# Kernel tuning notes

Hardware: AMD Instinct MI355X
Metric: run time of the kernel (lower is better)

Reference implementation:

```python
import jax, jax.numpy as jnp
import numpy as np

INPUT_DIM = 16
LW = 128          # layerwidth
NB_LAYERS = 4
NB_X = 4096
NB_THETA = 128
PARAM_COUNT = INPUT_DIM * LW + LW + (NB_LAYERS - 1) * (LW * LW + LW) + LW + 1  # 51841


def setup_inputs() -> dict:
    k1, k2 = jax.random.split(jax.random.key(0))
    x = jax.random.normal(k1, (NB_X, INPUT_DIM), dtype=jnp.float32)
    theta = jax.random.normal(k2, (NB_THETA, PARAM_COUNT), dtype=jnp.float32)
    return {"x": x, "theta": theta}


def reference(x, theta):
    # x: [nb_x, input_dim], theta: [nb_theta, param_count]
    t = theta.shape[0]
    off = 0
    # first layer: W0 [t, LW, INPUT_DIM], b0 [t, LW]
    W0 = theta[:, off:off + INPUT_DIM * LW].reshape(t, LW, INPUT_DIM); off += INPUT_DIM * LW
    b0 = theta[:, off:off + LW]; off += LW
    h = jnp.tanh(jnp.einsum('thi,xi->txh', W0, x) + b0[:, None, :])  # [t, nb_x, LW]
    # hidden layers
    for _ in range(NB_LAYERS - 1):
        W = theta[:, off:off + LW * LW].reshape(t, LW, LW); off += LW * LW
        b = theta[:, off:off + LW]; off += LW
        h = jnp.tanh(jnp.einsum('tho,txo->txh', W, h) + b[:, None, :])
    # output layer: Wl [t, LW], bl [t, 1]
    Wl = theta[:, off:off + LW]; off += LW
    bl = theta[:, off:off + 1]
    out = jnp.einsum('th,txh->tx', Wl, h)[..., None] + bl[:, None, :]  # [t, nb_x, 1]
    return out
```

## Files before the change

### kernel.cpp

```cpp
#include <hip/hip_runtime.h>


#define IND      16
#define THREADS  1024
#define PARAMS   51841
#define SCALE    2.8853900817779268f

#define WS_W0    12582912
#define WS_SC    (WS_W0 + 128 * 8192)
#define WS_X     (WS_SC + 128 * 4096)
#define WS_XLO   (WS_X + 131072)
#define WS_TOTAL (WS_X + 262144)


#define LDS_B    98304
#define LDS_WL   (LDS_B + 1536)
#define LDS_SZ   (LDS_B + 2064)

typedef _Float16 f16x8 __attribute__((ext_vector_type(8)));
typedef _Float16 f16x4 __attribute__((ext_vector_type(4)));
typedef float    f32x16 __attribute__((ext_vector_type(16)));
typedef float    f32x4v __attribute__((ext_vector_type(4)));
typedef unsigned u32x2  __attribute__((ext_vector_type(2)));

union U4 { unsigned u[4]; f16x8 v; };

__device__ __forceinline__ unsigned tanh2pk(float z0, float z1) {
    const float e0 = __builtin_amdgcn_exp2f(z0);
    const float e1 = __builtin_amdgcn_exp2f(z1);
    const float y0 = __builtin_fmaf(__builtin_amdgcn_rcpf(1.0f + e0), -2.0f, 1.0f);
    const float y1 = __builtin_fmaf(__builtin_amdgcn_rcpf(1.0f + e1), -2.0f, 1.0f);
    return __builtin_bit_cast(unsigned, __builtin_amdgcn_cvt_pkrtz(y0, y1));
}

#define MFMA(A, B, C) __builtin_amdgcn_mfma_f32_32x32x16_f16((A), (B), (C), 0, 0, 0)

__device__ __forceinline__ void gload16(const void* g, void* l) {
    __builtin_amdgcn_global_load_lds(
        (const __attribute__((address_space(1))) void*)g,
        (__attribute__((address_space(3))) void*)l, 16, 0, 0);
}

__device__ __forceinline__ void conv8(const float* __restrict__ s, char* hidst,
                                      char* lodst, float scale) {
    float v[8];
    *reinterpret_cast<float4*>(v)     = *reinterpret_cast<const float4*>(s);
    *reinterpret_cast<float4*>(v + 4) = *reinterpret_cast<const float4*>(s + 4);
    f16x8 hi, lo;
#pragma unroll
    for (int i = 0; i < 8; ++i) {
        const float sv = v[i] * scale;
        hi[i] = (_Float16)sv;
        lo[i] = (_Float16)(sv - (float)hi[i]);
    }
    *reinterpret_cast<f16x8*>(hidst) = hi;
    *reinterpret_cast<f16x8*>(lodst) = lo;
}

__global__ __launch_bounds__(256)
void prep_kernel(const float* __restrict__ theta, const float* __restrict__ xin,
                 char* __restrict__ ws)
{
    const int b = blockIdx.x, tid = threadIdx.x;
    if (b < 3072) {
        const int t = b / 24, rem = b % 24, li = rem >> 3, hblk = rem & 7;
        const int h  = hblk * 16 + (tid >> 4);
        const int kc = (tid >> 1) & 7, kh = tid & 1;
        const float* src = theta + (size_t)t * PARAMS + 2176 + li * 16512
                         + h * 128 + kc * 16 + kh * 8;
        float v[8];
        *reinterpret_cast<float4*>(v)     = *reinterpret_cast<const float4*>(src);
        *reinterpret_cast<float4*>(v + 4) = *reinterpret_cast<const float4*>(src + 4);
        f16x8 p;
#pragma unroll
        for (int i = 0; i < 8; ++i) p[i] = (_Float16)(v[i] * SCALE);
        char* img = ws + ((size_t)(t * 3 + li) << 15);
        *reinterpret_cast<f16x8*>(img + ((h >> 5) * 8 + kc) * 1024
                                      + (kh * 32 + (h & 31)) * 16) = p;
    } else if (b < 3136) {
        const int gid = (b - 3072) * 256 + tid;
        const int t = gid >> 7, h = gid & 127;
        const float* src = theta + (size_t)t * PARAMS + h * IND;
        char* dst = ws + WS_W0 + (size_t)t * 8192 + h * 32;
        conv8(src,     dst,      dst + 4096,      SCALE);
        conv8(src + 8, dst + 16, dst + 4096 + 16, SCALE);
    } else if (b < 3264) {
        const int t = b - 3136;
        const float* th = theta + (size_t)t * PARAMS;
        float* base = reinterpret_cast<float*>(ws + WS_SC + (size_t)t * 4096);
        if (tid < 128) base[tid] = SCALE * th[2048 + tid];
        for (int k = tid; k < 384; k += 256)
            base[128 + k] = SCALE * th[2176 + (k >> 7) * 16512 + 16384 + (k & 127)];
        if (tid < 128) base[512 + tid] = th[51712 + tid];
        if (tid == 0)  base[640] = th[51840];
    } else {
        const int row = (b - 3264) * 256 + tid;
        const float* src = xin + (size_t)row * IND;
        char* hid = ws + WS_X   + (size_t)row * 32;
        char* lod = ws + WS_XLO + (size_t)row * 32;
        conv8(src,     hid,      lod,      1.0f);
        conv8(src + 8, hid + 16, lod + 16, 1.0f);
    }
}

__global__ __launch_bounds__(THREADS, 4)
void mlp_main(const char* __restrict__ ws, float* __restrict__ out)
{
    __shared__ __align__(16) char sL[LDS_SZ];

    const int tid = threadIdx.x, bid = blockIdx.x;
    const int sw  = (bid & 7) * 128 + (bid >> 3);
    const int t   = sw >> 3, xt = sw & 7;
    const int lane = tid & 63, w = tid >> 6, r31 = lane & 31, khalf = lane >> 5;
    const int bpa  = (lane ^ 32) << 2;
    (void)bpa;

    const float* __restrict__ wsc = reinterpret_cast<const float*>(
        ws + WS_SC + (size_t)t * 4096);

    {
        const char* img = ws + ((size_t)(t * 3) << 15);
#pragma unroll
        for (int c = 0; c < 6; ++c) {
            const int o = (c * 1024 + tid) * 16;
            gload16(img + o, sL + o);
        }
    }
    if (tid < 513)
        *reinterpret_cast<float*>(sL + LDS_B + tid * 4) = wsc[128 + tid];

    auto asm2 = [&](const unsigned* P0, const unsigned* P1, f16x8* dst) {
#pragma unroll
        for (int j = 0; j < 2; ++j) {
#if __has_builtin(__builtin_amdgcn_permlane32_swap)
            const u32x2 r0 = __builtin_amdgcn_permlane32_swap(
                P0[2 * j], P0[2 * j + 1], false, false);
            const u32x2 r1 = __builtin_amdgcn_permlane32_swap(
                P1[2 * j], P1[2 * j + 1], false, false);
            U4 u;
            u.u[0] = r0[0]; u.u[1] = r1[0]; u.u[2] = r0[1]; u.u[3] = r1[1];
#else
            const unsigned s0 = khalf ? P0[2 * j] : P0[2 * j + 1];
            const unsigned s1 = khalf ? P1[2 * j] : P1[2 * j + 1];
            const unsigned q0 = (unsigned)__builtin_amdgcn_ds_bpermute(bpa, (int)s0);
            const unsigned q1 = (unsigned)__builtin_amdgcn_ds_bpermute(bpa, (int)s1);
            U4 u;
            u.u[0] = khalf ? q0 : P0[2 * j];
            u.u[1] = khalf ? q1 : P1[2 * j];
            u.u[2] = khalf ? P0[2 * j + 1] : q0;
            u.u[3] = khalf ? P1[2 * j + 1] : q1;
#endif
            dst[j] = u.v;
        }
    };
    auto pack2 = [&](const f32x16& a, f16x8* dst) {
        unsigned P0[4], P1[4];
#pragma unroll
        for (int g = 0; g < 4; ++g) {
            P0[g] = tanh2pk(a[4 * g + 0], a[4 * g + 1]);
            P1[g] = tanh2pk(a[4 * g + 2], a[4 * g + 3]);
        }
        asm2(P0, P1, dst);
    };
    auto biasin = [&](f32x16& a, const char* btab, int tt) {
#pragma unroll
        for (int g = 0; g < 4; ++g) {
            const f32x4v bv = *reinterpret_cast<const f32x4v*>(
                btab + (tt * 32 + g * 8) * 4 + khalf * 16);
            a[4 * g + 0] = bv[0]; a[4 * g + 1] = bv[1];
            a[4 * g + 2] = bv[2]; a[4 * g + 3] = bv[3];
        }
    };
    auto mfma8 = [&](f32x16& a, const char* wimg, int tt,
                     const f16x8* in0, const f16x8* in1) {
#pragma unroll
        for (int kc = 0; kc < 8; ++kc) {
            const f16x8 av = *reinterpret_cast<const f16x8*>(
                wimg + (tt * 8 + kc) * 1024 + lane * 16);
            a = MFMA(av, kc < 4 ? in0[kc] : in1[kc - 4], a);
        }
    };
    auto inter8 = [&](f32x16& a, const char* wimg, int tt,
                      const f16x8* in0, const f16x8* in1,
                      const f32x16& src, unsigned* P0, unsigned* P1) {
#pragma unroll
        for (int kc = 0; kc < 8; ++kc) {
            const f16x8 av = *reinterpret_cast<const f16x8*>(
                wimg + (tt * 8 + kc) * 1024 + lane * 16);
            a = MFMA(av, kc < 4 ? in0[kc] : in1[kc - 4], a);
            if (!(kc & 1)) {
                const int g = kc >> 1;
                P0[g] = tanh2pk(src[4 * g + 0], src[4 * g + 1]);
                P1[g] = tanh2pk(src[4 * g + 2], src[4 * g + 3]);
            }
        }
    };
    auto inter8f = [&](f32x16& a, const char* wimg, int tt,
                       const f16x8* in0, const f16x8* in1,
                       const f32x16& src, int tts, float& s) {
#pragma unroll
        for (int kc = 0; kc < 8; ++kc) {
            const f16x8 av = *reinterpret_cast<const f16x8*>(
                wimg + (tt * 8 + kc) * 1024 + lane * 16);
            a = MFMA(av, kc < 4 ? in0[kc] : in1[kc - 4], a);
            if (!(kc & 1)) {
                const int g = kc >> 1;
                const f32x4v wv = *reinterpret_cast<const f32x4v*>(
                    sL + LDS_WL + (tts * 32 + g * 8) * 4 + khalf * 16);
#pragma unroll
                for (int q = 0; q < 4; ++q) {
                    const float z = src[4 * g + q];
                    const float e = __builtin_amdgcn_exp2f(z);
                    const float y = __builtin_fmaf(
                        __builtin_amdgcn_rcpf(1.0f + e), -2.0f, 1.0f);
                    s = __builtin_fmaf(y, wv[q], s);
                }
            }
        }
    };
    auto fdot = [&](const f32x16& a, int tt, float& s) {
#pragma unroll
        for (int g = 0; g < 4; ++g) {
            const f32x4v wv = *reinterpret_cast<const f32x4v*>(
                sL + LDS_WL + (tt * 32 + g * 8) * 4 + khalf * 16);
#pragma unroll
            for (int q = 0; q < 4; ++q) {
                const float z = a[4 * g + q];
                const float e = __builtin_amdgcn_exp2f(z);
                const float y = __builtin_fmaf(
                    __builtin_amdgcn_rcpf(1.0f + e), -2.0f, 1.0f);
                s = __builtin_fmaf(y, wv[q], s);
            }
        }
    };

    f16x8 FA[4], FB[4], FC[4];
    {
        const char* w0i = ws + WS_W0 + (size_t)t * 8192;
        const int ro = r31 * 32 + khalf * 16;
        const int xrow = (xt * 512 + w * 32) * 32;
        const f16x8 B0h = *reinterpret_cast<const f16x8*>(ws + WS_X   + xrow + ro);
        const f16x8 B0l = *reinterpret_cast<const f16x8*>(ws + WS_XLO + xrow + ro);
        auto l0tile = [&](f32x16& a, int tt) {
#pragma unroll
            for (int g = 0; g < 4; ++g) {
                const f32x4v bv = *reinterpret_cast<const f32x4v*>(
                    wsc + tt * 32 + g * 8 + khalf * 4);
                a[4 * g + 0] = bv[0]; a[4 * g + 1] = bv[1];
                a[4 * g + 2] = bv[2]; a[4 * g + 3] = bv[3];
            }
            const f16x8 Ah = *reinterpret_cast<const f16x8*>(w0i + tt * 1024 + ro);
            const f16x8 Al = *reinterpret_cast<const f16x8*>(w0i + 4096 + tt * 1024 + ro);
            a = MFMA(Al, B0h, a);
            a = MFMA(Ah, B0l, a);
            a = MFMA(Ah, B0h, a);
        };
        f32x16 c0, c1;
        l0tile(c0, 0); l0tile(c1, 1);
        pack2(c0, &FA[0]); pack2(c1, &FA[2]);
        l0tile(c0, 2); l0tile(c1, 3);
        pack2(c0, &FB[0]); pack2(c1, &FB[2]);
    }
    __syncthreads();

    auto hidden = [&](const char* wimg, const char* btab,
                      f16x8* in0, f16x8* in1, f16x8* out0) {
        f32x16 c0, c1, c2, c3;
        __builtin_amdgcn_s_setprio(1);
        biasin(c0, btab, 0); mfma8(c0, wimg, 0, in0, in1);
        biasin(c1, btab, 1); mfma8(c1, wimg, 1, in0, in1);
        {
            unsigned P0[4], P1[4];
            biasin(c2, btab, 2);
            inter8(c2, wimg, 2, in0, in1, c0, P0, P1);
            asm2(P0, P1, out0 + 0);
        }
        {
            unsigned P0[4], P1[4];
            biasin(c3, btab, 3);
            inter8(c3, wimg, 3, in0, in1, c1, P0, P1);
            asm2(P0, P1, out0 + 2);
        }
        __builtin_amdgcn_s_setprio(0);
        pack2(c2, in1 + 0);
        pack2(c3, in1 + 2);
    };

    hidden(sL,         sL + LDS_B,        FA, FB, FC);
    hidden(sL + 32768, sL + LDS_B + 512,  FC, FB, FA);

    float s = 0.0f;
    {
        const char* wimg = sL + 65536;
        const char* btab = sL + LDS_B + 1024;
        f32x16 c0, c1, c2, c3;
        __builtin_amdgcn_s_setprio(1);
        biasin(c0, btab, 0); mfma8(c0, wimg, 0, FA, FB);
        biasin(c1, btab, 1); mfma8(c1, wimg, 1, FA, FB);
        biasin(c2, btab, 2); inter8f(c2, wimg, 2, FA, FB, c0, 0, s);
        biasin(c3, btab, 3); inter8f(c3, wimg, 3, FA, FB, c1, 1, s);
        __builtin_amdgcn_s_setprio(0);
        fdot(c2, 2, s);
        fdot(c3, 3, s);
    }
    const float sp = __builtin_bit_cast(float,
        __builtin_amdgcn_ds_bpermute(bpa, __builtin_bit_cast(int, s)));
    const float res = s + sp + *reinterpret_cast<const float*>(sL + LDS_WL + 512);
    if (!khalf) out[(size_t)t * 4096 + xt * 512 + w * 32 + r31] = res;
}

__global__ __launch_bounds__(256, 1)
void mlp_kernel_fb(const float* __restrict__ xin,
                   const float* __restrict__ theta,
                   float* __restrict__ out)
{
    __shared__ __align__(16) _Float16 sH   [128 * 128];
    __shared__ __align__(16) _Float16 sWhi [128 * 128];
    __shared__ __align__(16) _Float16 sWlo [128 * 128];
    __shared__ __align__(16) _Float16 sX0hi[128 * IND];
    __shared__ __align__(16) _Float16 sX0lo[128 * IND];
    __shared__ __align__(16) _Float16 sW0hi[128 * IND];
    __shared__ __align__(16) _Float16 sW0lo[128 * IND];
    __shared__ float sB[2][128];
    __shared__ float sWl[129];

    const int tid = threadIdx.x;
    const int bid = blockIdx.x;
    const int sw  = (bid & 7) * 512 + (bid >> 3);
    const int t   = sw >> 5;
    const int xt  = sw & 31;
    const float* __restrict__ th = theta + (size_t)t * PARAMS;
    const float* __restrict__ xg = xin   + (size_t)xt * (128 * IND);

#pragma unroll
    for (int j = 0; j < 2; ++j) {
        const int flat = j * 1024 + tid * 4;
        const float4 v = *reinterpret_cast<const float4*>(xg + flat);
        _Float16 h0 = (_Float16)v.x, h1 = (_Float16)v.y, h2 = (_Float16)v.z, h3 = (_Float16)v.w;
        f16x4 ph = {h0, h1, h2, h3};
        f16x4 pl = {(_Float16)(v.x - (float)h0), (_Float16)(v.y - (float)h1),
                    (_Float16)(v.z - (float)h2), (_Float16)(v.w - (float)h3)};
        *reinterpret_cast<f16x4*>(&sX0hi[flat]) = ph;
        *reinterpret_cast<f16x4*>(&sX0lo[flat]) = pl;
    }
#pragma unroll
    for (int j = 0; j < 2; ++j) {
        const int flat = j * 1024 + tid * 4;
        const float a0 = th[flat], a1 = th[flat + 1], a2 = th[flat + 2], a3 = th[flat + 3];
        _Float16 h0 = (_Float16)a0, h1 = (_Float16)a1, h2 = (_Float16)a2, h3 = (_Float16)a3;
        f16x4 ph = {h0, h1, h2, h3};
        f16x4 pl = {(_Float16)(a0 - (float)h0), (_Float16)(a1 - (float)h1),
                    (_Float16)(a2 - (float)h2), (_Float16)(a3 - (float)h3)};
        *reinterpret_cast<f16x4*>(&sW0hi[flat]) = ph;
        *reinterpret_cast<f16x4*>(&sW0lo[flat]) = pl;
    }
    if (tid < 128) sB[0][tid] = th[IND * 128 + tid];
    __syncthreads();

    const int lane  = tid & 63;
    const int w     = tid >> 6;
    const int r31   = lane & 31;
    const int khalf = lane >> 5;
    const int hb    = (w >> 1) * 64;
    const int xb    = (w & 1) * 64;
    const int hA0 = hb + r31,  hA1 = hb + 32 + r31;
    const int xB0 = xb + r31,  xB1 = xb + 32 + r31;
    const int swzA0 = (hA0 & 15) << 4, swzA1 = (hA1 & 15) << 4;
    const int swzB0 = (xB0 & 15) << 4, swzB1 = (xB1 & 15) << 4;

    f32x16 acc[2][2];

    {
        const int kb = khalf * 16;
        f16x8 ah[2], al[2], bh[2], bl[2];
        ah[0] = *reinterpret_cast<const f16x8*>((const char*)sW0hi + hA0 * 32 + kb);
        ah[1] = *reinterpret_cast<const f16x8*>((const char*)sW0hi + hA1 * 32 + kb);
        al[0] = *reinterpret_cast<const f16x8*>((const char*)sW0lo + hA0 * 32 + kb);
        al[1] = *reinterpret_cast<const f16x8*>((const char*)sW0lo + hA1 * 32 + kb);
        bh[0] = *reinterpret_cast<const f16x8*>((const char*)sX0hi + xB0 * 32 + kb);
        bh[1] = *reinterpret_cast<const f16x8*>((const char*)sX0hi + xB1 * 32 + kb);
        bl[0] = *reinterpret_cast<const f16x8*>((const char*)sX0lo + xB0 * 32 + kb);
        bl[1] = *reinterpret_cast<const f16x8*>((const char*)sX0lo + xB1 * 32 + kb);
#pragma unroll
        for (int tt = 0; tt < 2; ++tt)
#pragma unroll
            for (int tx = 0; tx < 2; ++tx) {
                f32x16 a;
#pragma unroll
                for (int i = 0; i < 16; ++i) a[i] = 0.0f;
                a = MFMA(al[tt], bh[tx], a);
                a = MFMA(ah[tt], bl[tx], a);
                a = MFMA(ah[tt], bh[tx], a);
                acc[tt][tx] = a;
            }
    }

    auto epilogue = [&](const float* __restrict__ bb) {
#pragma unroll
        for (int tt = 0; tt < 2; ++tt)
#pragma unroll
            for (int tx = 0; tx < 2; ++tx) {
                const int xw  = xb + tx * 32 + r31;
                const int swz = (xw & 15) << 4;
#pragma unroll
                for (int g = 0; g < 4; ++g) {
                    const int hbase = hb + tt * 32 + g * 8 + khalf * 4;
                    f16x4 pk;
#pragma unroll
                    for (int q = 0; q < 4; ++q) {
                        const float v = acc[tt][tx][g * 4 + q] + bb[hbase + q];
                        pk[q] = (_Float16)(1.0f - 2.0f * __builtin_amdgcn_rcpf(
                            __builtin_amdgcn_exp2f(v * 2.8853900817779268f) + 1.0f));
                    }
                    *reinterpret_cast<f16x4*>((char*)sH + xw * 256 + ((hbase * 2) ^ swz)) = pk;
                }
            }
    };

    for (int l = 0; l < 3; ++l) {
        __syncthreads();
        const float* __restrict__ wsrc = th + 2176 + l * 16512;
#pragma unroll
        for (int j = 0; j < 16; ++j) {
            const int flat = j * 1024 + tid * 4;
            const int hrow = flat >> 7;
            const int o    = flat & 127;
            const float a0 = wsrc[flat], a1 = wsrc[flat + 1], a2 = wsrc[flat + 2], a3 = wsrc[flat + 3];
            _Float16 h0 = (_Float16)a0, h1 = (_Float16)a1, h2 = (_Float16)a2, h3 = (_Float16)a3;
            f16x4 ph = {h0, h1, h2, h3};
            f16x4 pl = {(_Float16)(a0 - (float)h0), (_Float16)(a1 - (float)h1),
                        (_Float16)(a2 - (float)h2), (_Float16)(a3 - (float)h3)};
            const int boff = hrow * 256 + ((o * 2) ^ ((hrow & 15) << 4));
            *reinterpret_cast<f16x4*>((char*)sWhi + boff) = ph;
            *reinterpret_cast<f16x4*>((char*)sWlo + boff) = pl;
        }
        if (tid < 128) sB[(l + 1) & 1][tid] = wsrc[128 * 128 + tid];
        if (l == 2) {
            if (tid < 128) sWl[tid] = th[51712 + tid];
            if (tid == 128) sWl[128] = th[51840];
        }

        epilogue(sB[l & 1]);
        __syncthreads();

#pragma unroll
        for (int tt = 0; tt < 2; ++tt)
#pragma unroll
            for (int tx = 0; tx < 2; ++tx)
#pragma unroll
                for (int i = 0; i < 16; ++i) acc[tt][tx][i] = 0.0f;
#pragma unroll
        for (int kc = 0; kc < 8; ++kc) {
            const int kb = kc * 32 + khalf * 16;
            f16x8 ah[2], al[2], bv[2];
            ah[0] = *reinterpret_cast<const f16x8*>((const char*)sWhi + hA0 * 256 + (kb ^ swzA0));
            ah[1] = *reinterpret_cast<const f16x8*>((const char*)sWhi + hA1 * 256 + (kb ^ swzA1));
            al[0] = *reinterpret_cast<const f16x8*>((const char*)sWlo + hA0 * 256 + (kb ^ swzA0));
            al[1] = *reinterpret_cast<const f16x8*>((const char*)sWlo + hA1 * 256 + (kb ^ swzA1));
            bv[0] = *reinterpret_cast<const f16x8*>((const char*)sH   + xB0 * 256 + (kb ^ swzB0));
            bv[1] = *reinterpret_cast<const f16x8*>((const char*)sH   + xB1 * 256 + (kb ^ swzB1));
#pragma unroll
            for (int tt = 0; tt < 2; ++tt)
#pragma unroll
                for (int tx = 0; tx < 2; ++tx) {
                    acc[tt][tx] = MFMA(al[tt], bv[tx], acc[tt][tx]);
                    acc[tt][tx] = MFMA(ah[tt], bv[tx], acc[tt][tx]);
                }
        }
    }

    __syncthreads();
    epilogue(sB[1]);
    __syncthreads();

    if (tid < 128) {
        const int r   = tid;
        const int swz = (r & 15) << 4;
        float s = 0.0f;
#pragma unroll
        for (int c = 0; c < 16; ++c) {
            const int hc = (c + r) & 15;
            const f16x8 hv = *reinterpret_cast<const f16x8*>(
                (const char*)sH + r * 256 + ((hc * 16) ^ swz));
#pragma unroll
            for (int q = 0; q < 8; ++q) s += (float)hv[q] * sWl[hc * 8 + q];
        }
        out[(size_t)t * 4096 + (size_t)xt * 128 + r] = s + sWl[128];
    }
}

extern "C" void kernel_launch(void* const* d_in, const int* in_sizes, int n_in,
                              void* d_out, int out_size, void* d_ws, size_t ws_size,
                              hipStream_t stream)
{
    const float* x     = (const float*)d_in[0];
    const float* theta = (const float*)d_in[1];
    float* out = (float*)d_out;

    if (ws_size >= (size_t)WS_TOTAL) {
        prep_kernel<<<dim3(3280), dim3(256), 0, stream>>>(theta, x, (char*)d_ws);
        mlp_main<<<dim3(1024), dim3(THREADS), 0, stream>>>((const char*)d_ws, out);
    } else {
        mlp_kernel_fb<<<dim3(4096), dim3(256), 0, stream>>>(x, theta, out);
    }
}
```

Measured before the change: 91.69 us.

## Pipeline tanh of each output tile under the next tile's MFMAs across layers

Restructures the hidden and final layers so each 32-row output tile's tanh/pack runs interleaved with the MFMAs of the next tile. The last tile of each layer is carried over as raw accumulators into the next layer's first tile, and its activation is computed while that tile's first MFMAs run. This shrinks the exposed tanh tail that previously sat after two full MFMA tiles. In exchange it keeps an extra f32x16 accumulator live across layers, which raises register pressure, and it makes the data dependencies between layers more intricate.

```diff
diff --git a/kernel.cpp b/kernel.cpp
--- a/kernel.cpp
+++ b/kernel.cpp
@@ -21,6 +21,7 @@
 typedef _Float16 f16x4 __attribute__((ext_vector_type(4)));
 typedef float    f32x16 __attribute__((ext_vector_type(16)));
 typedef float    f32x4v __attribute__((ext_vector_type(4)));
+typedef float    f32x2v __attribute__((ext_vector_type(2)));
 typedef unsigned u32x2  __attribute__((ext_vector_type(2)));
 
 union U4 { unsigned u[4]; f16x8 v; };
@@ -171,51 +172,61 @@
             a[4 * g + 2] = bv[2]; a[4 * g + 3] = bv[3];
         }
     };
-    auto mfma8 = [&](f32x16& a, const char* wimg, int tt,
-                     const f16x8* in0, const f16x8* in1) {
+    auto tile0p = [&](f32x16& a, const char* wimg, f16x8* G, const f32x16& src) {
+        unsigned P0[4], P1[4];
+#pragma unroll
+        for (int kc = 0; kc < 4; ++kc) {
+            const f16x8 av = *reinterpret_cast<const f16x8*>(
+                wimg + kc * 1024 + lane * 16);
+            a = MFMA(av, G[kc], a);
+            P0[kc] = tanh2pk(src[4 * kc + 0], src[4 * kc + 1]);
+            P1[kc] = tanh2pk(src[4 * kc + 2], src[4 * kc + 3]);
+        }
+        {
+            const f16x8 a4 = *reinterpret_cast<const f16x8*>(wimg + 4 * 1024 + lane * 16);
+            a = MFMA(a4, G[4], a);
+            const f16x8 a5 = *reinterpret_cast<const f16x8*>(wimg + 5 * 1024 + lane * 16);
+            a = MFMA(a5, G[5], a);
+        }
+        asm2(P0, P1, G + 6);
+        {
+            const f16x8 a6 = *reinterpret_cast<const f16x8*>(wimg + 6 * 1024 + lane * 16);
+            a = MFMA(a6, G[6], a);
+            const f16x8 a7 = *reinterpret_cast<const f16x8*>(wimg + 7 * 1024 + lane * 16);
+            a = MFMA(a7, G[7], a);
+        }
+    };
+    auto inter8p = [&](f32x16& a, const char* wimg, int tt, const f16x8* G,
+                       const f32x16& src, f16x8* dst2) {
+        unsigned P0[4], P1[4];
 #pragma unroll
         for (int kc = 0; kc < 8; ++kc) {
             const f16x8 av = *reinterpret_cast<const f16x8*>(
                 wimg + (tt * 8 + kc) * 1024 + lane * 16);
-            a = MFMA(av, kc < 4 ? in0[kc] : in1[kc - 4], a);
-        }
-    };
-    auto inter8 = [&](f32x16& a, const char* wimg, int tt,
-                      const f16x8* in0, const f16x8* in1,
-                      const f32x16& src, unsigned* P0, unsigned* P1) {
+            a = MFMA(av, G[kc], a);
+            const int g = kc >> 1;
+            if (!(kc & 1)) P0[g] = tanh2pk(src[4 * g + 0], src[4 * g + 1]);
+            else           P1[g] = tanh2pk(src[4 * g + 2], src[4 * g + 3]);
+        }
+        asm2(P0, P1, dst2);
+    };
+    auto inter8d = [&](f32x16& a, const char* wimg, int tt, const f16x8* G,
+                       const f32x16& src, int tts, float& s) {
 #pragma unroll
         for (int kc = 0; kc < 8; ++kc) {
             const f16x8 av = *reinterpret_cast<const f16x8*>(
                 wimg + (tt * 8 + kc) * 1024 + lane * 16);
-            a = MFMA(av, kc < 4 ? in0[kc] : in1[kc - 4], a);
-            if (!(kc & 1)) {
-                const int g = kc >> 1;
-                P0[g] = tanh2pk(src[4 * g + 0], src[4 * g + 1]);
-                P1[g] = tanh2pk(src[4 * g + 2], src[4 * g + 3]);
-            }
-        }
-    };
-    auto inter8f = [&](f32x16& a, const char* wimg, int tt,
-                       const f16x8* in0, const f16x8* in1,
-                       const f32x16& src, int tts, float& s) {
-#pragma unroll
-        for (int kc = 0; kc < 8; ++kc) {
-            const f16x8 av = *reinterpret_cast<const f16x8*>(
-                wimg + (tt * 8 + kc) * 1024 + lane * 16);
-            a = MFMA(av, kc < 4 ? in0[kc] : in1[kc - 4], a);
-            if (!(kc & 1)) {
-                const int g = kc >> 1;
-                const f32x4v wv = *reinterpret_cast<const f32x4v*>(
-                    sL + LDS_WL + (tts * 32 + g * 8) * 4 + khalf * 16);
-#pragma unroll
-                for (int q = 0; q < 4; ++q) {
-                    const float z = src[4 * g + q];
-                    const float e = __builtin_amdgcn_exp2f(z);
-                    const float y = __builtin_fmaf(
-                        __builtin_amdgcn_rcpf(1.0f + e), -2.0f, 1.0f);
-                    s = __builtin_fmaf(y, wv[q], s);
-                }
-            }
+            a = MFMA(av, G[kc], a);
+            const int j = 2 * kc;
+            const int g = j >> 2, q = j & 3;
+            const f32x2v wv = *reinterpret_cast<const f32x2v*>(
+                sL + LDS_WL + (tts * 32 + g * 8 + khalf * 4 + q) * 4);
+            const float e0 = __builtin_amdgcn_exp2f(src[j]);
+            s = __builtin_fmaf(__builtin_fmaf(
+                    __builtin_amdgcn_rcpf(1.0f + e0), -2.0f, 1.0f), wv[0], s);
+            const float e1 = __builtin_amdgcn_exp2f(src[j + 1]);
+            s = __builtin_fmaf(__builtin_fmaf(
+                    __builtin_amdgcn_rcpf(1.0f + e1), -2.0f, 1.0f), wv[1], s);
         }
     };
     auto fdot = [&](const f32x16& a, int tt, float& s) {
@@ -225,8 +236,7 @@
                 sL + LDS_WL + (tt * 32 + g * 8) * 4 + khalf * 16);
 #pragma unroll
             for (int q = 0; q < 4; ++q) {
-                const float z = a[4 * g + q];
-                const float e = __builtin_amdgcn_exp2f(z);
+                const float e = __builtin_amdgcn_exp2f(a[4 * g + q]);
                 const float y = __builtin_fmaf(
                     __builtin_amdgcn_rcpf(1.0f + e), -2.0f, 1.0f);
                 s = __builtin_fmaf(y, wv[q], s);
@@ -234,7 +244,8 @@
         }
     };
 
-    f16x8 FA[4], FB[4], FC[4];
+    f16x8 G[8], N[8];
+    f32x16 pc;
     {
         const char* w0i = ws + WS_W0 + (size_t)t * 8192;
         const int ro = r31 * 32 + khalf * 16;
@@ -257,51 +268,39 @@
         };
         f32x16 c0, c1;
         l0tile(c0, 0); l0tile(c1, 1);
-        pack2(c0, &FA[0]); pack2(c1, &FA[2]);
-        l0tile(c0, 2); l0tile(c1, 3);
-        pack2(c0, &FB[0]); pack2(c1, &FB[2]);
+        pack2(c0, G + 0); pack2(c1, G + 2);
+        l0tile(c0, 2); l0tile(pc, 3);
+        pack2(c0, G + 4);
     }
     __syncthreads();
 
     auto hidden = [&](const char* wimg, const char* btab,
-                      f16x8* in0, f16x8* in1, f16x8* out0) {
+                      f16x8* Gc, f16x8* Nn) {
         f32x16 c0, c1, c2, c3;
         __builtin_amdgcn_s_setprio(1);
-        biasin(c0, btab, 0); mfma8(c0, wimg, 0, in0, in1);
-        biasin(c1, btab, 1); mfma8(c1, wimg, 1, in0, in1);
-        {
-            unsigned P0[4], P1[4];
-            biasin(c2, btab, 2);
-            inter8(c2, wimg, 2, in0, in1, c0, P0, P1);
-            asm2(P0, P1, out0 + 0);
-        }
-        {
-            unsigned P0[4], P1[4];
-            biasin(c3, btab, 3);
-            inter8(c3, wimg, 3, in0, in1, c1, P0, P1);
-            asm2(P0, P1, out0 + 2);
-        }
+        biasin(c0, btab, 0); tile0p(c0, wimg, Gc, pc);
+        biasin(c1, btab, 1); inter8p(c1, wimg, 1, Gc, c0, Nn + 0);
+        biasin(c2, btab, 2); inter8p(c2, wimg, 2, Gc, c1, Nn + 2);
+        biasin(c3, btab, 3); inter8p(c3, wimg, 3, Gc, c2, Nn + 4);
         __builtin_amdgcn_s_setprio(0);
-        pack2(c2, in1 + 0);
-        pack2(c3, in1 + 2);
-    };
-
-    hidden(sL,         sL + LDS_B,        FA, FB, FC);
-    hidden(sL + 32768, sL + LDS_B + 512,  FC, FB, FA);
+        pc = c3;
+    };
+
+    hidden(sL,         sL + LDS_B,       G, N);
+    hidden(sL + 32768, sL + LDS_B + 512, N, G);
 
     float s = 0.0f;
     {
         const char* wimg = sL + 65536;
         const char* btab = sL + LDS_B + 1024;
-        f32x16 c0, c1, c2, c3;
+        f32x16 c0f, c1f, c2f, c3f;
         __builtin_amdgcn_s_setprio(1);
-        biasin(c0, btab, 0); mfma8(c0, wimg, 0, FA, FB);
-        biasin(c1, btab, 1); mfma8(c1, wimg, 1, FA, FB);
-        biasin(c2, btab, 2); inter8f(c2, wimg, 2, FA, FB, c0, 0, s);
-        biasin(c3, btab, 3); inter8f(c3, wimg, 3, FA, FB, c1, 1, s);
+        biasin(c0f, btab, 0); tile0p(c0f, wimg, G, pc);
+        biasin(c1f, btab, 1); inter8d(c1f, wimg, 1, G, c0f, 0, s);
+        biasin(c2f, btab, 2); inter8d(c2f, wimg, 2, G, c1f, 1, s);
+        biasin(c3f, btab, 3); inter8d(c3f, wimg, 3, G, c2f, 2, s);
         __builtin_amdgcn_s_setprio(0);
-        fdot(c2, 2, s);
-        fdot(c3, 3, s);
+        fdot(c3f, 3, s);
     }
     const float sp = __builtin_bit_cast(float,
         __builtin_amdgcn_ds_bpermute(bpa, __builtin_bit_cast(int, s)));
```

Result: no change. 91.90 us (+0.2%).
